# Kernel tuning notes

Measured on AMD Instinct MI355X. Metric: run time of the kernel, lower is better.

Reference implementation:

```python
import jax, jax.numpy as jnp
import numpy as np

H_STEPS = 30 * 24 * 12
HID = 128
BATCH = 16


def setup_inputs() -> dict:
    key = jax.random.key(0)
    ks = jax.random.split(key, 16)
    s = 1.0 / np.sqrt(HID)  # PyTorch LSTM/Linear init scale
    u = lambda k, shape: jax.random.uniform(k, shape, jnp.float32, -s, s)
    return {
        "y0": jax.random.normal(ks[0], (BATCH, 1, 1), jnp.float32),
        "h0": jax.random.normal(ks[1], (2, BATCH, HID), jnp.float32),
        "c0": jax.random.normal(ks[2], (2, BATCH, HID), jnp.float32),
        "W_ih0": u(ks[3], (4 * HID, 1)),
        "W_hh0": u(ks[4], (4 * HID, HID)),
        "b_ih0": u(ks[5], (4 * HID,)),
        "b_hh0": u(ks[6], (4 * HID,)),
        "W_ih1": u(ks[7], (4 * HID, HID)),
        "W_hh1": u(ks[8], (4 * HID, HID)),
        "b_ih1": u(ks[9], (4 * HID,)),
        "b_hh1": u(ks[10], (4 * HID,)),
        "fc_w": u(ks[11], (1, HID)),
        "fc_b": u(ks[12], (1,)),
    }


def _lstm_cell(x, h, c, Wi, Wh, bi, bh):
    # PyTorch gate order: i, f, g, o
    gates = x @ Wi.T + bi + h @ Wh.T + bh  # [B, 4H]
    i, f, g, o = jnp.split(gates, 4, axis=-1)
    c_new = jax.nn.sigmoid(f) * c + jax.nn.sigmoid(i) * jnp.tanh(g)
    h_new = jax.nn.sigmoid(o) * jnp.tanh(c_new)
    return h_new, c_new


def reference(y0, h0, c0, W_ih0, W_hh0, b_ih0, b_hh0,
              W_ih1, W_hh1, b_ih1, b_hh1, fc_w, fc_b):
    def step(carry, _):
        y, h0_, c0_, h1_, c1_ = carry  # y: [B,1]
        h0n, c0n = _lstm_cell(y, h0_, c0_, W_ih0, W_hh0, b_ih0, b_hh0)
        h1n, c1n = _lstm_cell(h0n, h1_, c1_, W_ih1, W_hh1, b_ih1, b_hh1)
        yn = h1n @ fc_w.T + fc_b  # [B,1]
        return (yn, h0n, c0n, h1n, c1n), yn

    carry0 = (y0[:, 0, :], h0[0], c0[0], h0[1], c0[1])
    _, ys = jax.lax.scan(step, carry0, None, length=H_STEPS)  # [H, B, 1]
    return jnp.transpose(ys, (1, 0, 2))  # [B, H, 1]
```

## Files before the change

kernel.cpp:

```cpp
#include <hip/hip_runtime.h>

#define HSTEPS 8640
#define HID 128
#define BATCH 16
#define NTHR 512
#define YRING 192
#define INV127 (1.0f / 127.0f)

typedef __attribute__((ext_vector_type(4))) int i32x4;

static __device__ __forceinline__ float sigm(float x) {
    return __builtin_amdgcn_rcpf(1.0f + __expf(-x));
}
template <int CTRL>
static __device__ __forceinline__ float dppmov(float x) {
    return __int_as_float(
        __builtin_amdgcn_mov_dpp(__float_as_int(x), CTRL, 0xF, 0xF, false));
}
static __device__ __forceinline__ float sum4(float x) {
    x += dppmov<0x121>(x);
    x += dppmov<0x122>(x);
    return x;
}
static __device__ __forceinline__ float red_wave(float x) {
    x += dppmov<0x121>(x);
    x += dppmov<0x122>(x);
    x += dppmov<0x124>(x);
    x += dppmov<0x128>(x);
    float t1 = __int_as_float(__builtin_amdgcn_update_dpp(
        0, __float_as_int(x), 0x142 , 0xA, 0xF, false));
    x += t1;
    float t2 = __int_as_float(__builtin_amdgcn_update_dpp(
        0, __float_as_int(x), 0x143 , 0xC, 0xF, false));
    x += t2;
    return x;
}
static __device__ __forceinline__ float maxwave(float x) {
    x = fmaxf(x, dppmov<0x121>(x));
    x = fmaxf(x, dppmov<0x122>(x));
    x = fmaxf(x, dppmov<0x124>(x));
    x = fmaxf(x, dppmov<0x128>(x));
    float t1 = __int_as_float(__builtin_amdgcn_update_dpp(
        0, __float_as_int(x), 0x142, 0xA, 0xF, false));
    x = fmaxf(x, t1);
    float t2 = __int_as_float(__builtin_amdgcn_update_dpp(
        0, __float_as_int(x), 0x143, 0xC, 0xF, false));
    x = fmaxf(x, t2);
    return x;
}
static __device__ __forceinline__ float swzx16(float x) {
    return __int_as_float(
        __builtin_amdgcn_ds_swizzle(__float_as_int(x), 0x401F));
}

static __device__ __forceinline__ int pack4(const float* v, float inv) {
    int a = (int)__builtin_rintf(v[0] * inv);
    int b = (int)__builtin_rintf(v[1] * inv);
    int c = (int)__builtin_rintf(v[2] * inv);
    int d = (int)__builtin_rintf(v[3] * inv);
    return (a & 0xff) | ((b & 0xff) << 8) | ((c & 0xff) << 16) |
           ((d & 0xff) << 24);
}

static __device__ __forceinline__ void quantrow(const float* rp, int grp,
                                                i32x4& f0, i32x4& f1,
                                                float& sw) {
    float v[32];
#pragma unroll
    for (int j = 0; j < 16; ++j) v[j] = rp[16 * grp + j];
#pragma unroll
    for (int j = 0; j < 16; ++j) v[16 + j] = rp[64 + 16 * grp + j];
    float mx = 1e-20f;
#pragma unroll
    for (int j = 0; j < 32; ++j) mx = fmaxf(mx, __builtin_fabsf(v[j]));
    mx = fmaxf(mx, swzx16(mx));
    mx = fmaxf(mx, __shfl_xor(mx, 32, 64));
    float inv = 127.0f / mx;
    sw = mx * INV127;
    f0 = i32x4{pack4(v, inv), pack4(v + 4, inv), pack4(v + 8, inv),
               pack4(v + 12, inv)};
    f1 = i32x4{pack4(v + 16, inv), pack4(v + 20, inv), pack4(v + 24, inv),
               pack4(v + 28, inv)};
}

static __device__ __forceinline__ void quantrow2(const float* rpA,
                                                 const float* rpB, int grp,
                                                 i32x4& a0, i32x4& a1,
                                                 i32x4& b0, i32x4& b1,
                                                 float& sw) {
    float vA[32], vB[32];
#pragma unroll
    for (int j = 0; j < 16; ++j) {
        vA[j] = rpA[16 * grp + j];
        vA[16 + j] = rpA[64 + 16 * grp + j];
        vB[j] = rpB[16 * grp + j];
        vB[16 + j] = rpB[64 + 16 * grp + j];
    }
    float mx = 1e-20f;
#pragma unroll
    for (int j = 0; j < 32; ++j) {
        mx = fmaxf(mx, __builtin_fabsf(vA[j]));
        mx = fmaxf(mx, __builtin_fabsf(vB[j]));
    }
    mx = fmaxf(mx, swzx16(mx));
    mx = fmaxf(mx, __shfl_xor(mx, 32, 64));
    float inv = 127.0f / mx;
    sw = mx * INV127;
    a0 = i32x4{pack4(vA, inv), pack4(vA + 4, inv), pack4(vA + 8, inv),
               pack4(vA + 12, inv)};
    a1 = i32x4{pack4(vA + 16, inv), pack4(vA + 20, inv), pack4(vA + 24, inv),
               pack4(vA + 28, inv)};
    b0 = i32x4{pack4(vB, inv), pack4(vB + 4, inv), pack4(vB + 8, inv),
               pack4(vB + 12, inv)};
    b1 = i32x4{pack4(vB + 16, inv), pack4(vB + 20, inv), pack4(vB + 24, inv),
               pack4(vB + 28, inv)};
}

#define ROWOFF(T) \
    ((size_t)(128 * ((T) >> 1) + 16 * (2 * gw + ((T) & 1)) + ln15) * HID)

#define CH2(Q, A0, A1, FA, FB)                                                \
    Q = __builtin_amdgcn_mfma_i32_16x16x64_i8((A0), FA, zqi, 0, 0, 0);        \
    Q = __builtin_amdgcn_mfma_i32_16x16x64_i8((A1), FB, (Q), 0, 0, 0);
#define CH2C(Q, A0, A1, FA, FB)                                               \
    Q = __builtin_amdgcn_mfma_i32_16x16x64_i8((A0), FA, (Q), 0, 0, 0);        \
    Q = __builtin_amdgcn_mfma_i32_16x16x64_i8((A1), FB, (Q), 0, 0, 0);

__global__ __launch_bounds__(NTHR, 2) void lstm2_kernel(
    const float* __restrict__ y0, const float* __restrict__ h0in,
    const float* __restrict__ c0in, const float* __restrict__ Wih0,
    const float* __restrict__ Whh0, const float* __restrict__ bih0,
    const float* __restrict__ bhh0, const float* __restrict__ Wih1,
    const float* __restrict__ Whh1, const float* __restrict__ bih1,
    const float* __restrict__ bhh1, const float* __restrict__ fcw,
    const float* __restrict__ fcb, float* __restrict__ out) {
    const int b = blockIdx.x;
    const int t = threadIdx.x;
    const int wv = t >> 6;
    const int ln = t & 63;
    const int grp = ln >> 4;
    const int ln15 = ln & 15;
    const int gw = wv & 3;
    const bool isX = wv < 4;
    const int jj = ln >> 5;
    const bool isBt = (ln & 16) != 0;
    const int e = 32 * gw + 16 * jj + ln15;
    const float foldc = isBt ? 2.0f : 1.0f;
    const int g1 = isBt ? 2 : 0;

    __shared__ __align__(16) char hsm8[512];
    __shared__ float ypartbuf[4];
    __shared__ float maxb[8];
    __shared__ float ybuf[YRING];

    const i32x4 zqi = {0, 0, 0, 0};

    i32x4 Fq0 = zqi, Fq1 = zqi, Fq2 = zqi, Fq3 = zqi, Fq4 = zqi, Fq5 = zqi,
          Fq6 = zqi, Fq7 = zqi, Fq8 = zqi, Fq9 = zqi, Fq10 = zqi, Fq11 = zqi,
          Fq12 = zqi, Fq13 = zqi, Fq14 = zqi, Fq15 = zqi, Fq16 = zqi,
          Fq17 = zqi, Fq18 = zqi, Fq19 = zqi, Fq20 = zqi, Fq21 = zqi,
          Fq22 = zqi, Fq23 = zqi, Fq24 = zqi, Fq25 = zqi, Fq26 = zqi,
          Fq27 = zqi, Fq28 = zqi, Fq29 = zqi, Fq30 = zqi, Fq31 = zqi;
    i32x4 Q0 = zqi, Q1 = zqi, Q2 = zqi, Q3 = zqi, Q4 = zqi, Q5 = zqi,
          Q6 = zqi, Q7 = zqi;
    float B1c = 0, B2c = 0;
    float E1c = 0, E2c = 0;
    float SAb1 = 0, SAb2 = 0;
    float SAq1 = 0, SAq2 = 0;
    float HB1 = 0, HB2 = 0;
    float Cst = 0;

    if (isX) {
        float S0, S1, S2, S3, S4, S5, S6, S7;
        quantrow(Whh0 + ROWOFF(0), grp, Fq0, Fq1, S0);
        quantrow(Whh0 + ROWOFF(1), grp, Fq2, Fq3, S1);
        quantrow(Whh0 + ROWOFF(2), grp, Fq4, Fq5, S2);
        quantrow(Whh0 + ROWOFF(3), grp, Fq6, Fq7, S3);
        quantrow(Whh0 + ROWOFF(4), grp, Fq8, Fq9, S4);
        quantrow(Whh0 + ROWOFF(5), grp, Fq10, Fq11, S5);
        quantrow(Whh0 + ROWOFF(6), grp, Fq12, Fq13, S6);
        quantrow(Whh0 + ROWOFF(7), grp, Fq14, Fq15, S7);
        SAb1 = (isBt ? (jj ? S5 : S4) : (jj ? S1 : S0)) * foldc;
        SAb2 = isBt ? (jj ? S7 : S6) : (jj ? S3 : S2);
        B1c = (bih0[g1 * 128 + e] + bhh0[g1 * 128 + e]) * foldc;
        B2c = bih0[(g1 + 1) * 128 + e] + bhh0[(g1 + 1) * 128 + e];
        E1c = Wih0[g1 * 128 + e] * foldc;
        E2c = Wih0[(g1 + 1) * 128 + e];
        Cst = isBt ? 0.f : c0in[b * HID + e];
    } else {
        float S0, S1, S2, S3, S4, S5, S6, S7;
        quantrow2(Wih1 + ROWOFF(0), Whh1 + ROWOFF(0), grp, Fq0, Fq1, Fq16,
                  Fq17, S0);
        quantrow2(Wih1 + ROWOFF(1), Whh1 + ROWOFF(1), grp, Fq2, Fq3, Fq18,
                  Fq19, S1);
        quantrow2(Wih1 + ROWOFF(2), Whh1 + ROWOFF(2), grp, Fq4, Fq5, Fq20,
                  Fq21, S2);
        quantrow2(Wih1 + ROWOFF(3), Whh1 + ROWOFF(3), grp, Fq6, Fq7, Fq22,
                  Fq23, S3);
        quantrow2(Wih1 + ROWOFF(4), Whh1 + ROWOFF(4), grp, Fq8, Fq9, Fq24,
                  Fq25, S4);
        quantrow2(Wih1 + ROWOFF(5), Whh1 + ROWOFF(5), grp, Fq10, Fq11, Fq26,
                  Fq27, S5);
        quantrow2(Wih1 + ROWOFF(6), Whh1 + ROWOFF(6), grp, Fq12, Fq13, Fq28,
                  Fq29, S6);
        quantrow2(Wih1 + ROWOFF(7), Whh1 + ROWOFF(7), grp, Fq14, Fq15, Fq30,
                  Fq31, S7);
        SAb1 = (isBt ? (jj ? S5 : S4) : (jj ? S1 : S0)) * foldc;
        SAb2 = isBt ? (jj ? S7 : S6) : (jj ? S3 : S2);
        SAq1 = SAb1 * INV127;
        SAq2 = SAb2 * INV127;
        B1c = (bih1[g1 * 128 + e] + bhh1[g1 * 128 + e]) * foldc;
        B2c = bih1[(g1 + 1) * 128 + e] + bhh1[(g1 + 1) * 128 + e];
        E1c = isBt ? 0.f : fcw[e];
        Cst = isBt ? 0.f : c0in[(BATCH + b) * HID + e];
    }

    const float fcb_ = fcb[0];

    float hv_ = 0.f;
    if (t < 128) hv_ = h0in[b * HID + t];
    else if (t < 256) hv_ = h0in[(BATCH + b) * HID + (t - 128)];
    float am = maxwave(__builtin_fabsf(hv_));
    if (ln == 63) maxb[wv] = am;
    if (t < 4) ypartbuf[t] = (t == 0) ? (y0[b] - fcb_) : 0.0f;
    __syncthreads();
    const float bm0 = fmaxf(fmaxf(maxb[0], maxb[1]), 1e-20f);
    const float bm1 = fmaxf(fmaxf(maxb[2], maxb[3]), 1e-20f);
    if (t < 128)
        hsm8[t] = (char)(int)__builtin_rintf(hv_ * (127.0f / bm0));
    else if (t < 256)
        hsm8[256 + (t - 128)] = (char)(int)__builtin_rintf(hv_ * (127.0f / bm1));
    __syncthreads();

    float* outb = out + (size_t)b * HSTEPS;

    if (isX) {
        SAq1 = SAb1 * (bm0 * INV127);
        SAq2 = SAb2 * (bm0 * INV127);
        i32x4 a0 = *(const i32x4*)&hsm8[16 * grp];
        i32x4 a1 = *(const i32x4*)&hsm8[64 + 16 * grp];
        CH2(Q0, a0, a1, Fq0, Fq1) CH2(Q1, a0, a1, Fq2, Fq3)
        CH2(Q2, a0, a1, Fq4, Fq5) CH2(Q3, a0, a1, Fq6, Fq7)
        CH2(Q4, a0, a1, Fq8, Fq9) CH2(Q5, a0, a1, Fq10, Fq11)
        CH2(Q6, a0, a1, Fq12, Fq13) CH2(Q7, a0, a1, Fq14, Fq15)
    } else {
        i32x4 b0_ = *(const i32x4*)&hsm8[256 + 16 * grp];
        i32x4 b1_ = *(const i32x4*)&hsm8[256 + 64 + 16 * grp];
        i32x4 T0, T1, T2, T3, T4, T5, T6, T7;
        CH2(T0, b0_, b1_, Fq16, Fq17) CH2(T1, b0_, b1_, Fq18, Fq19)
        CH2(T2, b0_, b1_, Fq20, Fq21) CH2(T3, b0_, b1_, Fq22, Fq23)
        CH2(T4, b0_, b1_, Fq24, Fq25) CH2(T5, b0_, b1_, Fq26, Fq27)
        CH2(T6, b0_, b1_, Fq28, Fq29) CH2(T7, b0_, b1_, Fq30, Fq31)
        int a1s = isBt ? (jj ? T5[0] : T4[0]) : (jj ? T1[0] : T0[0]);
        int a2s = isBt ? (jj ? T7[0] : T6[0]) : (jj ? T3[0] : T2[0]);
        HB1 = SAb1 * (bm1 * INV127) * (float)a1s;
        HB2 = SAb2 * (bm1 * INV127) * (float)a2s;
        Q0 = zqi; Q1 = zqi; Q2 = zqi; Q3 = zqi;
        Q4 = zqi; Q5 = zqi; Q6 = zqi; Q7 = zqi;
    }

    int p = 0;
    int ys = 0;
    int flush_at = YRING;

#pragma unroll 1
    for (int s = 0; s < HSTEPS; ++s) {
        if (isX) {
            float yv = sum4(ypartbuf[ln & 3]) + fcb_;
            if (s > 0) {
                if (t == 0) ybuf[ys] = yv;
                ys = (ys == YRING - 1) ? 0 : ys + 1;
            }
            int a1 = isBt ? (jj ? Q5[0] : Q4[0]) : (jj ? Q1[0] : Q0[0]);
            int a2 = isBt ? (jj ? Q7[0] : Q6[0]) : (jj ? Q3[0] : Q2[0]);
            float G1 = __builtin_fmaf(SAq1, (float)a1,
                                      __builtin_fmaf(E1c, yv, B1c));
            float G2 = __builtin_fmaf(SAq2, (float)a2,
                                      __builtin_fmaf(E2c, yv, B2c));
            float v1 = sigm(G1);
            float v2 = sigm(G2);
            float tg = __builtin_fmaf(2.f, swzx16(v1), -1.f);
            Cst = __builtin_fmaf(v2, Cst, v1 * tg);
            float v3 = sigm(2.f * Cst);
            float th = __builtin_fmaf(2.f, v3, -1.f);
            float h0n = swzx16(v2) * th;
            if (!(ln & 16))
                hsm8[(p ^ 1) * 128 + e] =
                    (char)(int)__builtin_rintf(h0n * 127.0f);
            if (s == 0) {
                SAq1 = SAb1 * INV127;
                SAq2 = SAb2 * INV127;
            }
        } else if (s > 0) {
            const char* h1p = hsm8 + 256 + 128 * p + 16 * grp;
            i32x4 b0_ = *(const i32x4*)(h1p);
            i32x4 b1_ = *(const i32x4*)(h1p + 64);
            CH2(Q0, b0_, b1_, Fq16, Fq17) CH2(Q1, b0_, b1_, Fq18, Fq19)
            CH2(Q2, b0_, b1_, Fq20, Fq21) CH2(Q3, b0_, b1_, Fq22, Fq23)
            CH2(Q4, b0_, b1_, Fq24, Fq25) CH2(Q5, b0_, b1_, Fq26, Fq27)
            CH2(Q6, b0_, b1_, Fq28, Fq29) CH2(Q7, b0_, b1_, Fq30, Fq31)
        }
        __syncthreads();

        if (isX) {
            if (s == flush_at) {
                if (t < YRING) outb[flush_at - YRING + t] = ybuf[t];
                flush_at += YRING;
            }
            const char* h0np = hsm8 + (p ^ 1) * 128 + 16 * grp;
            i32x4 d0 = *(const i32x4*)(h0np);
            i32x4 d1 = *(const i32x4*)(h0np + 64);
            CH2(Q0, d0, d1, Fq0, Fq1) CH2(Q1, d0, d1, Fq2, Fq3)
            CH2(Q2, d0, d1, Fq4, Fq5) CH2(Q3, d0, d1, Fq6, Fq7)
            CH2(Q4, d0, d1, Fq8, Fq9) CH2(Q5, d0, d1, Fq10, Fq11)
            CH2(Q6, d0, d1, Fq12, Fq13) CH2(Q7, d0, d1, Fq14, Fq15)
        } else {
            __builtin_amdgcn_s_setprio(1);
            const char* h0np = hsm8 + (p ^ 1) * 128 + 16 * grp;
            i32x4 d0 = *(const i32x4*)(h0np);
            i32x4 d1 = *(const i32x4*)(h0np + 64);
            CH2C(Q0, d0, d1, Fq0, Fq1) CH2C(Q1, d0, d1, Fq2, Fq3)
            CH2C(Q2, d0, d1, Fq4, Fq5) CH2C(Q3, d0, d1, Fq6, Fq7)
            CH2C(Q4, d0, d1, Fq8, Fq9) CH2C(Q5, d0, d1, Fq10, Fq11)
            CH2C(Q6, d0, d1, Fq12, Fq13) CH2C(Q7, d0, d1, Fq14, Fq15)
            int a1 = isBt ? (jj ? Q5[0] : Q4[0]) : (jj ? Q1[0] : Q0[0]);
            int a2 = isBt ? (jj ? Q7[0] : Q6[0]) : (jj ? Q3[0] : Q2[0]);
            float H1 = __builtin_fmaf(SAq1, (float)a1, B1c + HB1);
            float H2 = __builtin_fmaf(SAq2, (float)a2, B2c + HB2);
            float v1 = sigm(H1);
            float v2 = sigm(H2);
            float tg = __builtin_fmaf(2.f, swzx16(v1), -1.f);
            Cst = __builtin_fmaf(v2, Cst, v1 * tg);
            float v3 = sigm(2.f * Cst);
            float th = __builtin_fmaf(2.f, v3, -1.f);
            float h1n = swzx16(v2) * th;
            __builtin_amdgcn_s_setprio(0);
            if (!(ln & 16))
                hsm8[256 + (p ^ 1) * 128 + e] =
                    (char)(int)__builtin_rintf(h1n * 127.0f);
            float part = red_wave(E1c * h1n);
            if (ln == 63) ypartbuf[gw] = part;
            if (s == 0) {
                HB1 = 0.f;
                HB2 = 0.f;
            }
        }
        __syncthreads();
        p ^= 1;
    }

    if (isX) {
        float yv = sum4(ypartbuf[ln & 3]) + fcb_;
        if (t == 0) ybuf[YRING - 1] = yv;
    }
    __syncthreads();
    if (t < YRING) outb[HSTEPS - YRING + t] = ybuf[t];
}

extern "C" void kernel_launch(void* const* d_in, const int* in_sizes, int n_in,
                              void* d_out, int out_size, void* d_ws,
                              size_t ws_size, hipStream_t stream) {
    const float* y0 = (const float*)d_in[0];
    const float* h0 = (const float*)d_in[1];
    const float* c0 = (const float*)d_in[2];
    const float* Wih0 = (const float*)d_in[3];
    const float* Whh0 = (const float*)d_in[4];
    const float* bih0 = (const float*)d_in[5];
    const float* bhh0 = (const float*)d_in[6];
    const float* Wih1 = (const float*)d_in[7];
    const float* Whh1 = (const float*)d_in[8];
    const float* bih1 = (const float*)d_in[9];
    const float* bhh1 = (const float*)d_in[10];
    const float* fcw = (const float*)d_in[11];
    const float* fcb = (const float*)d_in[12];
    float* out = (float*)d_out;

    lstm2_kernel<<<dim3(BATCH), dim3(NTHR), 0, stream>>>(
        y0, h0, c0, Wih0, Whh0, bih0, bhh0, Wih1, Whh1, bih1, bhh1, fcw, fcb,
        out);
}
```

Measured before the change: 6.083 ms.

## Split LSTM gate work over sixteen waves with per-unit gate ownership

Doubles the block to 1024 threads so each wave owns 16 hidden units across all four gates. This cuts each wave's serial MFMA chain from eight accumulators to four and removes the cross-lane swizzles that paired gates between lanes. The output-projection reduction shrinks to a 16-lane DPP sum read at lane 0; with shift-right DPP the full sum lands in lane 15, so the value taken may be wrong. The launch bound rises to four blocks, which could force a tight VGPR cap and spills of the register-resident int8 weights, and every step now has 16-wave barriers.

```diff
diff --git a/kernel.cpp b/kernel.cpp
--- a/kernel.cpp
+++ b/kernel.cpp
@@ -3,7 +3,7 @@
 #define HSTEPS 8640
 #define HID 128
 #define BATCH 16
-#define NTHR 512
+#define NTHR 1024
 #define YRING 192
 #define INV127 (1.0f / 127.0f)
 
@@ -17,22 +17,17 @@
     return __int_as_float(
         __builtin_amdgcn_mov_dpp(__float_as_int(x), CTRL, 0xF, 0xF, false));
 }
-static __device__ __forceinline__ float sum4(float x) {
+static __device__ __forceinline__ float sum8(float x) {
     x += dppmov<0x121>(x);
     x += dppmov<0x122>(x);
+    x += dppmov<0x124>(x);
     return x;
 }
-static __device__ __forceinline__ float red_wave(float x) {
+static __device__ __forceinline__ float sum16(float x) {
     x += dppmov<0x121>(x);
     x += dppmov<0x122>(x);
     x += dppmov<0x124>(x);
     x += dppmov<0x128>(x);
-    float t1 = __int_as_float(__builtin_amdgcn_update_dpp(
-        0, __float_as_int(x), 0x142 , 0xA, 0xF, false));
-    x += t1;
-    float t2 = __int_as_float(__builtin_amdgcn_update_dpp(
-        0, __float_as_int(x), 0x143 , 0xC, 0xF, false));
-    x += t2;
     return x;
 }
 static __device__ __forceinline__ float maxwave(float x) {
@@ -116,9 +111,6 @@
                pack4(vB + 28, inv)};
 }
 
-#define ROWOFF(T) \
-    ((size_t)(128 * ((T) >> 1) + 16 * (2 * gw + ((T) & 1)) + ln15) * HID)
-
 #define CH2(Q, A0, A1, FA, FB)                                                \
     Q = __builtin_amdgcn_mfma_i32_16x16x64_i8((A0), FA, zqi, 0, 0, 0);        \
     Q = __builtin_amdgcn_mfma_i32_16x16x64_i8((A1), FB, (Q), 0, 0, 0);
@@ -126,7 +118,7 @@
     Q = __builtin_amdgcn_mfma_i32_16x16x64_i8((A0), FA, (Q), 0, 0, 0);        \
     Q = __builtin_amdgcn_mfma_i32_16x16x64_i8((A1), FB, (Q), 0, 0, 0);
 
-__global__ __launch_bounds__(NTHR, 2) void lstm2_kernel(
+__global__ __launch_bounds__(NTHR, 4) void lstm2_kernel(
     const float* __restrict__ y0, const float* __restrict__ h0in,
     const float* __restrict__ c0in, const float* __restrict__ Wih0,
     const float* __restrict__ Whh0, const float* __restrict__ bih0,
@@ -140,79 +132,68 @@
     const int ln = t & 63;
     const int grp = ln >> 4;
     const int ln15 = ln & 15;
-    const int gw = wv & 3;
-    const bool isX = wv < 4;
-    const int jj = ln >> 5;
-    const bool isBt = (ln & 16) != 0;
-    const int e = 32 * gw + 16 * jj + ln15;
-    const float foldc = isBt ? 2.0f : 1.0f;
-    const int g1 = isBt ? 2 : 0;
+    const int gw = wv & 7;
+    const bool isX = wv < 8;
+    const int e = 16 * gw + ln15;
 
     __shared__ __align__(16) char hsm8[512];
-    __shared__ float ypartbuf[4];
-    __shared__ float maxb[8];
+    __shared__ float ypartbuf[8];
+    __shared__ float maxb[16];
     __shared__ float ybuf[YRING];
 
     const i32x4 zqi = {0, 0, 0, 0};
 
-    i32x4 Fq0 = zqi, Fq1 = zqi, Fq2 = zqi, Fq3 = zqi, Fq4 = zqi, Fq5 = zqi,
-          Fq6 = zqi, Fq7 = zqi, Fq8 = zqi, Fq9 = zqi, Fq10 = zqi, Fq11 = zqi,
-          Fq12 = zqi, Fq13 = zqi, Fq14 = zqi, Fq15 = zqi, Fq16 = zqi,
-          Fq17 = zqi, Fq18 = zqi, Fq19 = zqi, Fq20 = zqi, Fq21 = zqi,
-          Fq22 = zqi, Fq23 = zqi, Fq24 = zqi, Fq25 = zqi, Fq26 = zqi,
-          Fq27 = zqi, Fq28 = zqi, Fq29 = zqi, Fq30 = zqi, Fq31 = zqi;
-    i32x4 Q0 = zqi, Q1 = zqi, Q2 = zqi, Q3 = zqi, Q4 = zqi, Q5 = zqi,
-          Q6 = zqi, Q7 = zqi;
-    float B1c = 0, B2c = 0;
-    float E1c = 0, E2c = 0;
-    float SAb1 = 0, SAb2 = 0;
-    float SAq1 = 0, SAq2 = 0;
-    float HB1 = 0, HB2 = 0;
+    i32x4 FA0a = zqi, FA0b = zqi, FA1a = zqi, FA1b = zqi;
+    i32x4 FA2a = zqi, FA2b = zqi, FA3a = zqi, FA3b = zqi;
+    i32x4 FB0a = zqi, FB0b = zqi, FB1a = zqi, FB1b = zqi;
+    i32x4 FB2a = zqi, FB2b = zqi, FB3a = zqi, FB3b = zqi;
+    i32x4 Q0 = zqi, Q1 = zqi, Q2 = zqi, Q3 = zqi;
+
+    float S0 = 0, S1 = 0, S2 = 0, S3 = 0;
+    float SQ0 = 0, SQ1 = 0, SQ2 = 0, SQ3 = 0;
+    float B0c = 0, B1c = 0, B2c = 0, B3c = 0;
+    float E0c = 0, E1c = 0, E2c = 0, E3c = 0;
+    float H0c = 0, H1c = 0, H2c = 0, H3c = 0;
     float Cst = 0;
 
     if (isX) {
-        float S0, S1, S2, S3, S4, S5, S6, S7;
-        quantrow(Whh0 + ROWOFF(0), grp, Fq0, Fq1, S0);
-        quantrow(Whh0 + ROWOFF(1), grp, Fq2, Fq3, S1);
-        quantrow(Whh0 + ROWOFF(2), grp, Fq4, Fq5, S2);
-        quantrow(Whh0 + ROWOFF(3), grp, Fq6, Fq7, S3);
-        quantrow(Whh0 + ROWOFF(4), grp, Fq8, Fq9, S4);
-        quantrow(Whh0 + ROWOFF(5), grp, Fq10, Fq11, S5);
-        quantrow(Whh0 + ROWOFF(6), grp, Fq12, Fq13, S6);
-        quantrow(Whh0 + ROWOFF(7), grp, Fq14, Fq15, S7);
-        SAb1 = (isBt ? (jj ? S5 : S4) : (jj ? S1 : S0)) * foldc;
-        SAb2 = isBt ? (jj ? S7 : S6) : (jj ? S3 : S2);
-        B1c = (bih0[g1 * 128 + e] + bhh0[g1 * 128 + e]) * foldc;
-        B2c = bih0[(g1 + 1) * 128 + e] + bhh0[(g1 + 1) * 128 + e];
-        E1c = Wih0[g1 * 128 + e] * foldc;
-        E2c = Wih0[(g1 + 1) * 128 + e];
-        Cst = isBt ? 0.f : c0in[b * HID + e];
+        quantrow(Whh0 + (size_t)(e)*HID, grp, FA0a, FA0b, S0);
+        quantrow(Whh0 + (size_t)(128 + e) * HID, grp, FA1a, FA1b, S1);
+        quantrow(Whh0 + (size_t)(256 + e) * HID, grp, FA2a, FA2b, S2);
+        quantrow(Whh0 + (size_t)(384 + e) * HID, grp, FA3a, FA3b, S3);
+        B0c = bih0[e] + bhh0[e];
+        B1c = bih0[128 + e] + bhh0[128 + e];
+        B2c = 2.0f * (bih0[256 + e] + bhh0[256 + e]);
+        B3c = bih0[384 + e] + bhh0[384 + e];
+        E0c = Wih0[e];
+        E1c = Wih0[128 + e];
+        E2c = 2.0f * Wih0[256 + e];
+        E3c = Wih0[384 + e];
+        S2 *= 2.0f;
+        Cst = c0in[b * HID + e];
     } else {
-        float S0, S1, S2, S3, S4, S5, S6, S7;
-        quantrow2(Wih1 + ROWOFF(0), Whh1 + ROWOFF(0), grp, Fq0, Fq1, Fq16,
-                  Fq17, S0);
-        quantrow2(Wih1 + ROWOFF(1), Whh1 + ROWOFF(1), grp, Fq2, Fq3, Fq18,
-                  Fq19, S1);
-        quantrow2(Wih1 + ROWOFF(2), Whh1 + ROWOFF(2), grp, Fq4, Fq5, Fq20,
-                  Fq21, S2);
-        quantrow2(Wih1 + ROWOFF(3), Whh1 + ROWOFF(3), grp, Fq6, Fq7, Fq22,
-                  Fq23, S3);
-        quantrow2(Wih1 + ROWOFF(4), Whh1 + ROWOFF(4), grp, Fq8, Fq9, Fq24,
-                  Fq25, S4);
-        quantrow2(Wih1 + ROWOFF(5), Whh1 + ROWOFF(5), grp, Fq10, Fq11, Fq26,
-                  Fq27, S5);
-        quantrow2(Wih1 + ROWOFF(6), Whh1 + ROWOFF(6), grp, Fq12, Fq13, Fq28,
-                  Fq29, S6);
-        quantrow2(Wih1 + ROWOFF(7), Whh1 + ROWOFF(7), grp, Fq14, Fq15, Fq30,
-                  Fq31, S7);
-        SAb1 = (isBt ? (jj ? S5 : S4) : (jj ? S1 : S0)) * foldc;
-        SAb2 = isBt ? (jj ? S7 : S6) : (jj ? S3 : S2);
-        SAq1 = SAb1 * INV127;
-        SAq2 = SAb2 * INV127;
-        B1c = (bih1[g1 * 128 + e] + bhh1[g1 * 128 + e]) * foldc;
-        B2c = bih1[(g1 + 1) * 128 + e] + bhh1[(g1 + 1) * 128 + e];
-        E1c = isBt ? 0.f : fcw[e];
-        Cst = isBt ? 0.f : c0in[(BATCH + b) * HID + e];
+        quantrow2(Wih1 + (size_t)(e)*HID, Whh1 + (size_t)(e)*HID, grp, FA0a,
+                  FA0b, FB0a, FB0b, S0);
+        quantrow2(Wih1 + (size_t)(128 + e) * HID,
+                  Whh1 + (size_t)(128 + e) * HID, grp, FA1a, FA1b, FB1a,
+                  FB1b, S1);
+        quantrow2(Wih1 + (size_t)(256 + e) * HID,
+                  Whh1 + (size_t)(256 + e) * HID, grp, FA2a, FA2b, FB2a,
+                  FB2b, S2);
+        quantrow2(Wih1 + (size_t)(384 + e) * HID,
+                  Whh1 + (size_t)(384 + e) * HID, grp, FA3a, FA3b, FB3a,
+                  FB3b, S3);
+        B0c = bih1[e] + bhh1[e];
+        B1c = bih1[128 + e] + bhh1[128 + e];
+        B2c = 2.0f * (bih1[256 + e] + bhh1[256 + e]);
+        B3c = bih1[384 + e] + bhh1[384 + e];
+        S2 *= 2.0f;
+        SQ0 = S0 * INV127;
+        SQ1 = S1 * INV127;
+        SQ2 = S2 * INV127;
+        SQ3 = S3 * INV127;
+        E0c = fcw[e];
+        Cst = c0in[(BATCH + b) * HID + e];
     }
 
     const float fcb_ = fcb[0];
@@ -222,7 +203,7 @@
     else if (t < 256) hv_ = h0in[(BATCH + b) * HID + (t - 128)];
     float am = maxwave(__builtin_fabsf(hv_));
     if (ln == 63) maxb[wv] = am;
-    if (t < 4) ypartbuf[t] = (t == 0) ? (y0[b] - fcb_) : 0.0f;
+    if (t < 8) ypartbuf[t] = (t == 0) ? (y0[b] - fcb_) : 0.0f;
     __syncthreads();
     const float bm0 = fmaxf(fmaxf(maxb[0], maxb[1]), 1e-20f);
     const float bm1 = fmaxf(fmaxf(maxb[2], maxb[3]), 1e-20f);
@@ -235,28 +216,31 @@
     float* outb = out + (size_t)b * HSTEPS;
 
     if (isX) {
-        SAq1 = SAb1 * (bm0 * INV127);
-        SAq2 = SAb2 * (bm0 * INV127);
+        float s0i = bm0 * INV127;
+        SQ0 = S0 * s0i;
+        SQ1 = S1 * s0i;
+        SQ2 = S2 * s0i;
+        SQ3 = S3 * s0i;
         i32x4 a0 = *(const i32x4*)&hsm8[16 * grp];
         i32x4 a1 = *(const i32x4*)&hsm8[64 + 16 * grp];
-        CH2(Q0, a0, a1, Fq0, Fq1) CH2(Q1, a0, a1, Fq2, Fq3)
-        CH2(Q2, a0, a1, Fq4, Fq5) CH2(Q3, a0, a1, Fq6, Fq7)
-        CH2(Q4, a0, a1, Fq8, Fq9) CH2(Q5, a0, a1, Fq10, Fq11)
-        CH2(Q6, a0, a1, Fq12, Fq13) CH2(Q7, a0, a1, Fq14, Fq15)
+        CH2(Q0, a0, a1, FA0a, FA0b)
+        CH2(Q1, a0, a1, FA1a, FA1b)
+        CH2(Q2, a0, a1, FA2a, FA2b)
+        CH2(Q3, a0, a1, FA3a, FA3b)
     } else {
         i32x4 b0_ = *(const i32x4*)&hsm8[256 + 16 * grp];
         i32x4 b1_ = *(const i32x4*)&hsm8[256 + 64 + 16 * grp];
-        i32x4 T0, T1, T2, T3, T4, T5, T6, T7;
-        CH2(T0, b0_, b1_, Fq16, Fq17) CH2(T1, b0_, b1_, Fq18, Fq19)
-        CH2(T2, b0_, b1_, Fq20, Fq21) CH2(T3, b0_, b1_, Fq22, Fq23)
-        CH2(T4, b0_, b1_, Fq24, Fq25) CH2(T5, b0_, b1_, Fq26, Fq27)
-        CH2(T6, b0_, b1_, Fq28, Fq29) CH2(T7, b0_, b1_, Fq30, Fq31)
-        int a1s = isBt ? (jj ? T5[0] : T4[0]) : (jj ? T1[0] : T0[0]);
-        int a2s = isBt ? (jj ? T7[0] : T6[0]) : (jj ? T3[0] : T2[0]);
-        HB1 = SAb1 * (bm1 * INV127) * (float)a1s;
-        HB2 = SAb2 * (bm1 * INV127) * (float)a2s;
+        i32x4 T0, T1, T2, T3;
+        CH2(T0, b0_, b1_, FB0a, FB0b)
+        CH2(T1, b0_, b1_, FB1a, FB1b)
+        CH2(T2, b0_, b1_, FB2a, FB2b)
+        CH2(T3, b0_, b1_, FB3a, FB3b)
+        float s1i = bm1 * INV127;
+        H0c = S0 * s1i * (float)T0[0];
+        H1c = S1 * s1i * (float)T1[0];
+        H2c = S2 * s1i * (float)T2[0];
+        H3c = S3 * s1i * (float)T3[0];
         Q0 = zqi; Q1 = zqi; Q2 = zqi; Q3 = zqi;
-        Q4 = zqi; Q5 = zqi; Q6 = zqi; Q7 = zqi;
     }
 
     int p = 0;
@@ -266,39 +250,40 @@
 #pragma unroll 1
     for (int s = 0; s < HSTEPS; ++s) {
         if (isX) {
-            float yv = sum4(ypartbuf[ln & 3]) + fcb_;
+            float yv = sum8(ypartbuf[ln & 7]) + fcb_;
             if (s > 0) {
                 if (t == 0) ybuf[ys] = yv;
                 ys = (ys == YRING - 1) ? 0 : ys + 1;
             }
-            int a1 = isBt ? (jj ? Q5[0] : Q4[0]) : (jj ? Q1[0] : Q0[0]);
-            int a2 = isBt ? (jj ? Q7[0] : Q6[0]) : (jj ? Q3[0] : Q2[0]);
-            float G1 = __builtin_fmaf(SAq1, (float)a1,
+            float G0 = __builtin_fmaf(SQ0, (float)Q0[0],
+                                      __builtin_fmaf(E0c, yv, B0c));
+            float G1 = __builtin_fmaf(SQ1, (float)Q1[0],
                                       __builtin_fmaf(E1c, yv, B1c));
-            float G2 = __builtin_fmaf(SAq2, (float)a2,
+            float G2 = __builtin_fmaf(SQ2, (float)Q2[0],
                                       __builtin_fmaf(E2c, yv, B2c));
-            float v1 = sigm(G1);
-            float v2 = sigm(G2);
-            float tg = __builtin_fmaf(2.f, swzx16(v1), -1.f);
-            Cst = __builtin_fmaf(v2, Cst, v1 * tg);
-            float v3 = sigm(2.f * Cst);
-            float th = __builtin_fmaf(2.f, v3, -1.f);
-            float h0n = swzx16(v2) * th;
-            if (!(ln & 16))
+            float G3 = __builtin_fmaf(SQ3, (float)Q3[0],
+                                      __builtin_fmaf(E3c, yv, B3c));
+            float si = sigm(G0), sf = sigm(G1), so = sigm(G3);
+            float tg = __builtin_fmaf(2.f, sigm(G2), -1.f);
+            Cst = __builtin_fmaf(sf, Cst, si * tg);
+            float h0n = so * __builtin_fmaf(2.f, sigm(2.f * Cst), -1.f);
+            if (ln < 16)
                 hsm8[(p ^ 1) * 128 + e] =
                     (char)(int)__builtin_rintf(h0n * 127.0f);
             if (s == 0) {
-                SAq1 = SAb1 * INV127;
-                SAq2 = SAb2 * INV127;
+                SQ0 = S0 * INV127;
+                SQ1 = S1 * INV127;
+                SQ2 = S2 * INV127;
+                SQ3 = S3 * INV127;
             }
         } else if (s > 0) {
             const char* h1p = hsm8 + 256 + 128 * p + 16 * grp;
             i32x4 b0_ = *(const i32x4*)(h1p);
             i32x4 b1_ = *(const i32x4*)(h1p + 64);
-            CH2(Q0, b0_, b1_, Fq16, Fq17) CH2(Q1, b0_, b1_, Fq18, Fq19)
-            CH2(Q2, b0_, b1_, Fq20, Fq21) CH2(Q3, b0_, b1_, Fq22, Fq23)
-            CH2(Q4, b0_, b1_, Fq24, Fq25) CH2(Q5, b0_, b1_, Fq26, Fq27)
-            CH2(Q6, b0_, b1_, Fq28, Fq29) CH2(Q7, b0_, b1_, Fq30, Fq31)
+            CH2(Q0, b0_, b1_, FB0a, FB0b)
+            CH2(Q1, b0_, b1_, FB1a, FB1b)
+            CH2(Q2, b0_, b1_, FB2a, FB2b)
+            CH2(Q3, b0_, b1_, FB3a, FB3b)
         }
         __syncthreads();
 
@@ -310,39 +295,38 @@
             const char* h0np = hsm8 + (p ^ 1) * 128 + 16 * grp;
             i32x4 d0 = *(const i32x4*)(h0np);
             i32x4 d1 = *(const i32x4*)(h0np + 64);
-            CH2(Q0, d0, d1, Fq0, Fq1) CH2(Q1, d0, d1, Fq2, Fq3)
-            CH2(Q2, d0, d1, Fq4, Fq5) CH2(Q3, d0, d1, Fq6, Fq7)
-            CH2(Q4, d0, d1, Fq8, Fq9) CH2(Q5, d0, d1, Fq10, Fq11)
-            CH2(Q6, d0, d1, Fq12, Fq13) CH2(Q7, d0, d1, Fq14, Fq15)
+            CH2(Q0, d0, d1, FA0a, FA0b)
+            CH2(Q1, d0, d1, FA1a, FA1b)
+            CH2(Q2, d0, d1, FA2a, FA2b)
+            CH2(Q3, d0, d1, FA3a, FA3b)
         } else {
             __builtin_amdgcn_s_setprio(1);
             const char* h0np = hsm8 + (p ^ 1) * 128 + 16 * grp;
             i32x4 d0 = *(const i32x4*)(h0np);
             i32x4 d1 = *(const i32x4*)(h0np + 64);
-            CH2C(Q0, d0, d1, Fq0, Fq1) CH2C(Q1, d0, d1, Fq2, Fq3)
-            CH2C(Q2, d0, d1, Fq4, Fq5) CH2C(Q3, d0, d1, Fq6, Fq7)
-            CH2C(Q4, d0, d1, Fq8, Fq9) CH2C(Q5, d0, d1, Fq10, Fq11)
-            CH2C(Q6, d0, d1, Fq12, Fq13) CH2C(Q7, d0, d1, Fq14, Fq15)
-            int a1 = isBt ? (jj ? Q5[0] : Q4[0]) : (jj ? Q1[0] : Q0[0]);
-            int a2 = isBt ? (jj ? Q7[0] : Q6[0]) : (jj ? Q3[0] : Q2[0]);
-            float H1 = __builtin_fmaf(SAq1, (float)a1, B1c + HB1);
-            float H2 = __builtin_fmaf(SAq2, (float)a2, B2c + HB2);
-            float v1 = sigm(H1);
-            float v2 = sigm(H2);
-            float tg = __builtin_fmaf(2.f, swzx16(v1), -1.f);
-            Cst = __builtin_fmaf(v2, Cst, v1 * tg);
-            float v3 = sigm(2.f * Cst);
-            float th = __builtin_fmaf(2.f, v3, -1.f);
-            float h1n = swzx16(v2) * th;
+            CH2C(Q0, d0, d1, FA0a, FA0b)
+            CH2C(Q1, d0, d1, FA1a, FA1b)
+            CH2C(Q2, d0, d1, FA2a, FA2b)
+            CH2C(Q3, d0, d1, FA3a, FA3b)
+            float H0 = __builtin_fmaf(SQ0, (float)Q0[0], B0c + H0c);
+            float H1 = __builtin_fmaf(SQ1, (float)Q1[0], B1c + H1c);
+            float H2 = __builtin_fmaf(SQ2, (float)Q2[0], B2c + H2c);
+            float H3 = __builtin_fmaf(SQ3, (float)Q3[0], B3c + H3c);
+            float ti = sigm(H0), tf = sigm(H1), to = sigm(H3);
+            float tg1 = __builtin_fmaf(2.f, sigm(H2), -1.f);
+            Cst = __builtin_fmaf(tf, Cst, ti * tg1);
+            float h1n = to * __builtin_fmaf(2.f, sigm(2.f * Cst), -1.f);
             __builtin_amdgcn_s_setprio(0);
-            if (!(ln & 16))
+            if (ln < 16)
                 hsm8[256 + (p ^ 1) * 128 + e] =
                     (char)(int)__builtin_rintf(h1n * 127.0f);
-            float part = red_wave(E1c * h1n);
-            if (ln == 63) ypartbuf[gw] = part;
+            float part = sum16(E0c * h1n);
+            if (ln == 0) ypartbuf[gw] = part;
             if (s == 0) {
-                HB1 = 0.f;
-                HB2 = 0.f;
+                H0c = 0.f;
+                H1c = 0.f;
+                H2c = 0.f;
+                H3c = 0.f;
             }
         }
         __syncthreads();
@@ -350,7 +334,7 @@
     }
 
     if (isX) {
-        float yv = sum4(ypartbuf[ln & 3]) + fcb_;
+        float yv = sum8(ypartbuf[ln & 7]) + fcb_;
         if (t == 0) ybuf[YRING - 1] = yv;
     }
     __syncthreads();
```

New measurement: 7.465 ms. +22.7%, slower.
